# Performance work log

Hardware: AMD Instinct MI355X
Metric: run time of the kernel (lower is better)

Reference implementation:

```python
import jax, jax.numpy as jnp
import numpy as np

N_AGENTS = 32
BROADCAST = 1
HIDDEN = 64
R, T = 16, 512
D_IN = (N_AGENTS - 1) * (3 + BROADCAST)  # 124
D_OUT = 2 + BROADCAST  # 3


def setup_inputs() -> dict:
    key = jax.random.key(0)
    ks = jax.random.split(key, 8)
    runs = jax.random.normal(ks[0], (R, T, N_AGENTS, N_AGENTS - 1, 3), jnp.float32)
    # init_comm(): uniform(1, 2) of shape (broadcast, N) per run
    comm_init = jax.random.uniform(ks[1], (R, BROADCAST, N_AGENTS), jnp.float32, 1.0, 2.0)
    scale = 0.05  # keep tanh out of saturation
    w1 = jax.random.normal(ks[2], (HIDDEN, D_IN), jnp.float32) * scale
    b1 = jax.random.normal(ks[3], (HIDDEN,), jnp.float32) * scale
    w2 = jax.random.normal(ks[4], (HIDDEN, HIDDEN), jnp.float32) * scale
    b2 = jax.random.normal(ks[5], (HIDDEN,), jnp.float32) * scale
    w3 = jax.random.normal(ks[6], (D_OUT, HIDDEN), jnp.float32) * scale
    b3 = jax.random.normal(ks[7], (D_OUT,), jnp.float32) * scale
    return {"runs": runs, "comm_init": comm_init, "w1": w1, "b1": b1,
            "w2": w2, "b2": b2, "w3": w3, "b3": b3}


def reference(runs, comm_init, w1, b1, w2, b2, w3, b3):
    # runs: [R, T, N, N-1, 3]; comm_init: [R, broadcast, N]
    Rr, Tt, Nn = runs.shape[0], runs.shape[1], runs.shape[2]
    # skip_diag_strided: row i = all agent indices except i, in order
    n_closest = jnp.asarray(
        np.array([[j for j in range(Nn) if j != i] for i in range(Nn)]), jnp.int32)
    agent_ids = jnp.arange(Nn, dtype=jnp.int32)

    def snet(x):  # eval mode: dropout disabled
        h = jnp.tanh(x @ w1.T + b1)
        h = jnp.tanh(h @ w2.T + b2)
        return h @ w3.T + b3  # [2 + broadcast]

    def agent_step(comm, inp):
        xs_i, idx_i, i = inp  # xs_i: [N-1, 3], idx_i: [N-1]
        rel = comm[:, idx_i]  # [broadcast, N-1] gather of neighbor comm
        x = jnp.concatenate([xs_i.reshape(-1), rel.reshape(-1)])  # [D_IN]
        out = snet(x)
        # comm update is detached in torch (output[2:].detach().numpy())
        comm = comm.at[:, i].set(jax.lax.stop_gradient(out[2:]))
        return comm, out[:2]

    def t_step(comm, xs_t):  # sequential scatter-update across agents
        comm, ctrl = jax.lax.scan(agent_step, comm, (xs_t, n_closest, agent_ids))
        return comm, ctrl  # ctrl: [N, 2]

    def run_fn(run, c0):
        _, controls = jax.lax.scan(t_step, c0, run)  # [T, N, 2]
        return controls

    return jax.vmap(run_fn)(runs, comm_init)  # [R, T, N, 2]
```

## Files before the change

kernel.cpp:

```cpp
#include <hip/hip_runtime.h>


#define R_RUNS 16
#define T_STEPS 512
#define NA 32
#define HID 64
#define XS 93
#define DIN 124
#define STEPS_PER_RUN (T_STEPS * NA)
#define RTI_TOT (R_RUNS * STEPS_PER_RUN)

#define PRE1_OFF 65536
#define WS_NEEDED ((size_t)PRE1_OFF + (size_t)RTI_TOT * HID * 4 + 4096)

typedef _Float16 half2_t __attribute__((ext_vector_type(2)));
typedef unsigned int uint2v __attribute__((ext_vector_type(2)));

#if defined(__has_builtin)
#if __has_builtin(__builtin_amdgcn_permlane16_swap) && __has_builtin(__builtin_amdgcn_permlane32_swap)
#define HAVE_PLSWAP 1
#endif
#endif
#ifndef HAVE_PLSWAP
#define HAVE_PLSWAP 0
#endif

#if defined(__has_builtin)
#if __has_builtin(__builtin_amdgcn_exp2f)
#define EXPFN(x) __builtin_amdgcn_exp2f(x)
#define SC 2.8853900817779268f
#define HAVE_EXP2 1
#endif
#endif
#ifndef HAVE_EXP2
#define EXPFN(x) __expf(x)
#define SC 2.0f
#define HAVE_EXP2 0
#endif

__device__ __forceinline__ float fast_tanh(float x) {
  float e = __expf(2.f * x);
  return fmaf(-2.f, __builtin_amdgcn_rcpf(e + 1.f), 1.f);
}

__device__ __forceinline__ float dot2h(half2_t a, half2_t b, float c) {
#if __has_builtin(__builtin_amdgcn_fdot2)
  return __builtin_amdgcn_fdot2(a, b, c, false);
#else
  return fmaf((float)a.x, (float)b.x, fmaf((float)a.y, (float)b.y, c));
#endif
}

__device__ __forceinline__ half2_t bch(unsigned u) {
  return __builtin_bit_cast(half2_t, u);
}

#define DPP_ADD(x, ctrl, rmask) \
  (x) += __int_as_float(__builtin_amdgcn_update_dpp(0, __float_as_int(x), (ctrl), (rmask), 0xf, true))

__device__ __forceinline__ float wave64_sum_bcast(float x) {
  DPP_ADD(x, 0x111, 0xf);
  DPP_ADD(x, 0x112, 0xf);
  DPP_ADD(x, 0x114, 0xf);
  DPP_ADD(x, 0x118, 0xf);
  DPP_ADD(x, 0x142, 0xa);
  DPP_ADD(x, 0x143, 0xc);
  return __int_as_float(__builtin_amdgcn_readlane(__float_as_int(x), 63));
}

__device__ __forceinline__ float wave64_sum_all(float x) {
  DPP_ADD(x, 0xB1, 0xf);
  DPP_ADD(x, 0x4E, 0xf);
  DPP_ADD(x, 0x141, 0xf);
  DPP_ADD(x, 0x140, 0xf);
#if HAVE_PLSWAP
  uint2v p = __builtin_amdgcn_permlane16_swap(__float_as_uint(x), __float_as_uint(x), false, false);
  x = __uint_as_float(p[0]) + __uint_as_float(p[1]);
  p = __builtin_amdgcn_permlane32_swap(__float_as_uint(x), __float_as_uint(x), false, false);
  x = __uint_as_float(p[0]) + __uint_as_float(p[1]);
  return x;
#else
  DPP_ADD(x, 0x142, 0xa);
  DPP_ADD(x, 0x143, 0xc);
  return __int_as_float(__builtin_amdgcn_readlane(__float_as_int(x), 63));
#endif
}

__global__ void transpose_w1(const float* __restrict__ w1, float* __restrict__ w1T) {
  int idx = blockIdx.x * blockDim.x + threadIdx.x;
  if (idx < XS * HID) {
    int k = idx / HID, h = idx % HID;
    w1T[idx] = w1[h * DIN + k];
  }
}

__global__ __launch_bounds__(256) void pre1_kernel(
    const float* __restrict__ runs, const float* __restrict__ w1T,
    const float* __restrict__ b1, float* __restrict__ pre1) {
  const int wid = (blockIdx.x * 256 + threadIdx.x) >> 6;
  const int lane = threadIdx.x & 63;
  const float* xs = runs + (size_t)wid * XS;
  float a0 = b1[lane], a1 = 0.f, a2 = 0.f;
#pragma unroll 4
  for (int k = 0; k < 31; ++k) {
    a0 = fmaf(xs[3 * k],     w1T[(3 * k) * HID + lane],     a0);
    a1 = fmaf(xs[3 * k + 1], w1T[(3 * k + 1) * HID + lane], a1);
    a2 = fmaf(xs[3 * k + 2], w1T[(3 * k + 2) * HID + lane], a2);
  }
  pre1[(size_t)wid * HID + lane] = SC * ((a0 + a1) + a2);
}

__global__ __launch_bounds__(256) void out_kernel(
    const float* __restrict__ h2, const float* __restrict__ w3,
    const float* __restrict__ b3, float* __restrict__ out) {
  const int rti = blockIdx.x * 256 + threadIdx.x;
  const float4* hv4 = (const float4*)(h2 + (size_t)rti * HID);
  const float4* w0v = (const float4*)w3;
  const float4* w1v = (const float4*)(w3 + HID);
  float p00 = 0.f, p01 = 0.f, p02 = 0.f, p03 = 0.f;
  float p10 = 0.f, p11 = 0.f, p12 = 0.f, p13 = 0.f;
#pragma unroll
  for (int k = 0; k < 16; ++k) {
    float4 hv = hv4[k];
    float4 w0 = w0v[k];
    float4 w1r = w1v[k];
    p00 = fmaf(w0.x, hv.x, p00);  p01 = fmaf(w0.y, hv.y, p01);
    p02 = fmaf(w0.z, hv.z, p02);  p03 = fmaf(w0.w, hv.w, p03);
    p10 = fmaf(w1r.x, hv.x, p10); p11 = fmaf(w1r.y, hv.y, p11);
    p12 = fmaf(w1r.z, hv.z, p12); p13 = fmaf(w1r.w, hv.w, p13);
  }
  float o0 = ((p00 + p01) + (p02 + p03)) + b3[0];
  float o1 = ((p10 + p11) + (p12 + p13)) + b3[1];
  *(float2*)(out + (size_t)rti * 2) = make_float2(o0, o1);
}

__global__ __launch_bounds__(64, 1) void seq_kernel(
    const float* __restrict__ w1, const float* __restrict__ w2,
    const float* __restrict__ b2, const float* __restrict__ w3,
    const float* __restrict__ b3, const float* __restrict__ comm_init,
    float* pre1h2) {
  const int h = threadIdx.x;
  const int r = blockIdx.x;
  const int hb = h * 33;

  __shared__ float Asl[HID * 33];
  __shared__ float Bsl[HID * 33];
  __shared__ __align__(16) float commL[NA];
  __shared__ __align__(16) _Float16 h1s16[HID];
  __shared__ __align__(16) float pbuf[2][2048 + 64];

  for (int j = 0; j < 31; ++j) Asl[hb + j] = SC * w1[h * DIN + 93 + j];
  Asl[hb + 31] = 0.f;
  Asl[hb + 32] = 0.f;
  Bsl[hb] = 0.f;
  for (int j = 1; j < 32; ++j) Bsl[hb + j] = SC * w1[h * DIN + 92 + j];
  Bsl[hb + 32] = 0.f;

  const float4* w2v = (const float4*)(w2 + h * HID);
  const float4 r0 = w2v[0],  r1 = w2v[1],  r2 = w2v[2],  r3 = w2v[3];
  const float4 r4 = w2v[4],  r5 = w2v[5],  r6 = w2v[6],  r7 = w2v[7];
  const float4 r8 = w2v[8],  r9 = w2v[9],  r10 = w2v[10], r11 = w2v[11];
  const float4 r12 = w2v[12], r13 = w2v[13], r14 = w2v[14], r15 = w2v[15];
#define PK2S(n, f4) \
  const half2_t n##a = {(_Float16)(SC * (f4).x), (_Float16)(SC * (f4).y)}; \
  const half2_t n##b = {(_Float16)(SC * (f4).z), (_Float16)(SC * (f4).w)}
  PK2S(q0, r0);  PK2S(q1, r1);  PK2S(q2, r2);  PK2S(q3, r3);
  PK2S(q4, r4);  PK2S(q5, r5);  PK2S(q6, r6);  PK2S(q7, r7);
  PK2S(q8, r8);  PK2S(q9, r9);  PK2S(q10, r10); PK2S(q11, r11);
  PK2S(q12, r12); PK2S(q13, r13); PK2S(q14, r14); PK2S(q15, r15);
#undef PK2S

  const float b2s = SC * b2[h];
  const float w32h = w3[2 * HID + h];
  const float w32n2 = -2.f * w32h;
  const float b32 = b3[2];

  float commR = (h < NA) ? comm_init[r * NA + h] : 0.f;
  if (h < NA) commL[h] = commR;

  float* prow = pre1h2 + (size_t)r * STEPS_PER_RUN * HID;

  {
    const float4* s0 = (const float4*)prow;
    const float4* s1 = (const float4*)(prow + 2048);
    float4* d0 = (float4*)&pbuf[0][0];
    float4* d1 = (float4*)&pbuf[1][0];
#pragma unroll
    for (int j = 0; j < 8; ++j) d0[j * 64 + h] = s0[j * 64 + h];
#pragma unroll
    for (int j = 0; j < 8; ++j) d1[j * 64 + h] = s1[j * 64 + h];
  }

  for (int t = 0; t < T_STEPS; ++t) {
    float* pb = pbuf[t & 1];
    int tk = (t + 2 <= T_STEPS - 1) ? t + 2 : T_STEPS - 1;
    const float4* gsrc = (const float4*)(prow + (size_t)tk * 2048);
    float4 g0 = gsrc[0 * 64 + h], g1 = gsrc[1 * 64 + h];
    float4 g2 = gsrc[2 * 64 + h], g3 = gsrc[3 * 64 + h];
    float4 g4 = gsrc[4 * 64 + h], g5 = gsrc[5 * 64 + h];
    float4 g6 = gsrc[6 * 64 + h], g7 = gsrc[7 * 64 + h];

    const float4* cv4 = (const float4*)commL;
    float f0 = 0.f, f1 = 0.f, f2 = 0.f, f3 = 0.f;
#pragma unroll
    for (int q = 0; q < 8; ++q) {
      float4 c = cv4[q];
      f0 = fmaf(Bsl[hb + 4 * q + 0], c.x, f0);
      f1 = fmaf(Bsl[hb + 4 * q + 1], c.y, f1);
      f2 = fmaf(Bsl[hb + 4 * q + 2], c.z, f2);
      f3 = fmaf(Bsl[hb + 4 * q + 3], c.w, f3);
    }
    const float FB2 = (f0 + f1) + (f2 + f3);
    const float c0s = commR;
    float Q2 = 0.f, S2 = 0.f;
    float A2_c = Asl[hb];
    float E = pb[h] + FB2;
    float* h2t = prow + (size_t)t * 2048;

#pragma unroll 4
    for (int i = 0; i < NA; ++i) {
      float pf2_n = pb[(i + 1) * 64 + h];
      float A2_n = Asl[hb + i + 1];
      float B2_n = Bsl[hb + i + 1];
      float old_n = __int_as_float(__builtin_amdgcn_readlane(__float_as_int(c0s), i + 1));
      float e1 = EXPFN(E);
      float r1v = __builtin_amdgcn_rcpf(e1 + 1.f);
      float h1 = fmaf(-2.f, r1v, 1.f);
      h1s16[h] = (_Float16)h1;
      float S2n = fmaf(B2_n, old_n, S2);
      float Qb2 = fmaf(A2_c, b32, Q2);
      float H = pf2_n + (FB2 - S2n) + Qb2;
      const uint4* hv = (const uint4*)h1s16;
      uint4 X0 = hv[0], X1 = hv[1], X2 = hv[2], X3 = hv[3];
      uint4 X4 = hv[4], X5 = hv[5], X6 = hv[6], X7 = hv[7];
      float a0 = b2s, a1 = 0.f, a2 = 0.f, a3 = 0.f;
#define DOTB(Xq, qe, qo) \
      a0 = dot2h(qe##a, bch(Xq.x), a0); a1 = dot2h(qe##b, bch(Xq.y), a1); \
      a2 = dot2h(qo##a, bch(Xq.z), a2); a3 = dot2h(qo##b, bch(Xq.w), a3)
      DOTB(X0, q0, q1);   DOTB(X1, q2, q3);
      DOTB(X2, q4, q5);   DOTB(X3, q6, q7);
      DOTB(X4, q8, q9);   DOTB(X5, q10, q11);
      DOTB(X6, q12, q13); DOTB(X7, q14, q15);
#undef DOTB
      float y2 = (a0 + a1) + (a2 + a3);
      float e2 = EXPFN(y2);
      float r2v = __builtin_amdgcn_rcpf(e2 + 1.f);
      float xr = fmaf(w32n2, r2v, w32h);
      float csum = wave64_sum_all(xr);
      float h2v = fmaf(-2.f, r2v, 1.f);
      h2t[i * 64 + h] = h2v;
      float c_new = csum + b32;
      commR = (h == i) ? c_new : commR;
      E = fmaf(A2_c, csum, H);
      Q2 = fmaf(A2_c, csum, Qb2);
      S2 = S2n; A2_c = A2_n;
    }
    if (h < NA) commL[h] = commR;
    float4* pd = (float4*)pb;
    pd[0 * 64 + h] = g0; pd[1 * 64 + h] = g1;
    pd[2 * 64 + h] = g2; pd[3 * 64 + h] = g3;
    pd[4 * 64 + h] = g4; pd[5 * 64 + h] = g5;
    pd[6 * 64 + h] = g6; pd[7 * 64 + h] = g7;
  }
}

__global__ __launch_bounds__(64, 1) void seq_fused(
    const float* __restrict__ runs, const float* __restrict__ comm_init,
    const float* __restrict__ w1, const float* __restrict__ b1,
    const float* __restrict__ w2, const float* __restrict__ b2,
    const float* __restrict__ w3, const float* __restrict__ b3,
    float* __restrict__ out) {
  const int r = blockIdx.x;
  const int h = threadIdx.x;
  const int hb = h * 33;

  __shared__ float Asl[HID * 33];
  __shared__ float Bsl[HID * 33];
  __shared__ float commL[NA];
  __shared__ __align__(16) float h1s[HID];
  __shared__ float w1xs[XS * HID];
  __shared__ __align__(16) float xsl[96];

  for (int j = 0; j < 31; ++j) Asl[hb + j] = w1[h * DIN + 93 + j];
  Asl[hb + 31] = 0.f;
  Bsl[hb] = 0.f;
  for (int j = 1; j < 32; ++j) Bsl[hb + j] = w1[h * DIN + 92 + j];
  for (int k = 0; k < XS; ++k) w1xs[k * HID + h] = w1[h * DIN + k];

  float w2r[HID];
#pragma unroll
  for (int k = 0; k < HID; ++k) w2r[k] = w2[h * HID + k];
  const float b1h = b1[h];
  const float b2h = b2[h];
  const float w30h = w3[h], w31h = w3[HID + h], w32h = w3[2 * HID + h];
  const float b30 = b3[0], b31 = b3[1], b32 = b3[2];
  if (h < NA) commL[h] = comm_init[r * NA + h];

  const float* xbase = runs + (size_t)r * STEPS_PER_RUN * XS;
  float xa = xbase[h];
  float xb = (h < XS - 64) ? xbase[64 + h] : 0.f;
  float* outp = out + (size_t)r * STEPS_PER_RUN * 2;
  __syncthreads();

  int s = 0;
  for (int t = 0; t < T_STEPS; ++t) {
    float FB = 0.f;
#pragma unroll
    for (int j = 0; j < NA; ++j) FB = fmaf(Bsl[hb + j], commL[j], FB);
    float Q = 0.f, S = 0.f;
    for (int i = 0; i < NA; ++i, ++s) {
      int sn = s + 1; if (sn > STEPS_PER_RUN - 1) sn = STEPS_PER_RUN - 1;
      const float* xn = xbase + (size_t)sn * XS;
      xsl[h] = xa;
      if (h < XS - 64) xsl[64 + h] = xb;
      __syncthreads();
      float xa_n = xn[h];
      float xb_n = (h < XS - 64) ? xn[64 + h] : 0.f;
      float a0 = b1h, a1 = 0.f, a2 = 0.f;
#pragma unroll 4
      for (int k = 0; k < 31; ++k) {
        a0 = fmaf(xsl[3 * k],     w1xs[(3 * k) * HID + h],     a0);
        a1 = fmaf(xsl[3 * k + 1], w1xs[(3 * k + 1) * HID + h], a1);
        a2 = fmaf(xsl[3 * k + 2], w1xs[(3 * k + 2) * HID + h], a2);
      }
      float old_i = commL[i];
      S = fmaf(Bsl[hb + i], old_i, S);
      float h1 = fast_tanh(((a0 + a1) + a2) + FB + Q - S);
      h1s[h] = h1;
      __syncthreads();
      float c0 = b2h, c1 = 0.f, c2 = 0.f, c3 = 0.f;
      const float4* hv4 = (const float4*)h1s;
#pragma unroll
      for (int k4 = 0; k4 < 16; ++k4) {
        float4 hv = hv4[k4];
        c0 = fmaf(w2r[4 * k4 + 0], hv.x, c0);
        c1 = fmaf(w2r[4 * k4 + 1], hv.y, c1);
        c2 = fmaf(w2r[4 * k4 + 2], hv.z, c2);
        c3 = fmaf(w2r[4 * k4 + 3], hv.w, c3);
      }
      float h2 = fast_tanh((c0 + c1) + (c2 + c3));
      float o0 = wave64_sum_bcast(w30h * h2) + b30;
      float o1 = wave64_sum_bcast(w31h * h2) + b31;
      float c_new = wave64_sum_bcast(w32h * h2) + b32;
      if (h == 0) *(float2*)(outp + (size_t)s * 2) = make_float2(o0, o1);
      Q = fmaf(Asl[hb + i], c_new, Q);
      if (h == i) commL[h] = c_new;
      __syncthreads();
      xa = xa_n; xb = xb_n;
    }
  }
}

extern "C" void kernel_launch(void* const* d_in, const int* in_sizes, int n_in,
                              void* d_out, int out_size, void* d_ws, size_t ws_size,
                              hipStream_t stream) {
  const float* runs = (const float*)d_in[0];
  const float* comm_init = (const float*)d_in[1];
  const float* w1 = (const float*)d_in[2];
  const float* b1 = (const float*)d_in[3];
  const float* w2 = (const float*)d_in[4];
  const float* b2 = (const float*)d_in[5];
  const float* w3 = (const float*)d_in[6];
  const float* b3 = (const float*)d_in[7];
  float* out = (float*)d_out;

  if (ws_size >= WS_NEEDED) {
    float* w1T = (float*)d_ws;
    float* pre1 = (float*)((char*)d_ws + PRE1_OFF);
    hipLaunchKernelGGL(transpose_w1, dim3((XS * HID + 255) / 256), dim3(256), 0, stream,
                       w1, w1T);
    hipLaunchKernelGGL(pre1_kernel, dim3(RTI_TOT / 4), dim3(256), 0, stream,
                       runs, w1T, b1, pre1);
    hipLaunchKernelGGL(seq_kernel, dim3(R_RUNS), dim3(64), 0, stream,
                       w1, w2, b2, w3, b3, comm_init, pre1);
    hipLaunchKernelGGL(out_kernel, dim3(RTI_TOT / 256), dim3(256), 0, stream,
                       pre1, w3, b3, out);
  } else {
    hipLaunchKernelGGL(seq_fused, dim3(R_RUNS), dim3(64), 0, stream,
                       runs, comm_init, w1, b1, w2, b2, w3, b3, out);
  }
}
```

Measured before the change: 4.348 ms.

## Split layer-2 matvec across wave halves with permlane swap; batch pre1 rows

In the sequential kernel, each lane now computes partial dot products over only 32 of the 64 hidden inputs for two output rows: its own and its partner lane's (h^32). The halves are then combined with a permlane32 swap. This halves the per-step LDS reads of h1, the main cost on the serial critical path, in exchange for one cross-lane swap. Separately, the pre1 kernel keeps a float4-packed transposed w1 in registers and processes four rows per wave, which raises register use.

```diff
diff --git a/kernel.cpp b/kernel.cpp
--- a/kernel.cpp
+++ b/kernel.cpp
@@ -86,28 +86,41 @@
 #endif
 }
 
-__global__ void transpose_w1(const float* __restrict__ w1, float* __restrict__ w1T) {
+__global__ void transpose_w1(const float* __restrict__ w1, float* __restrict__ w1T4) {
   int idx = blockIdx.x * blockDim.x + threadIdx.x;
-  if (idx < XS * HID) {
-    int k = idx / HID, h = idx % HID;
-    w1T[idx] = w1[h * DIN + k];
-  }
-}
-
+  if (idx < 24 * HID * 4) {
+    int c = idx & 3, h = (idx >> 2) & 63, kk = idx >> 8;
+    int k = 4 * kk + c;
+    w1T4[idx] = (k < XS) ? w1[h * DIN + k] : 0.f;
+  }
+}
+
+#define PRE1_BATCH 4
 __global__ __launch_bounds__(256) void pre1_kernel(
-    const float* __restrict__ runs, const float* __restrict__ w1T,
+    const float* __restrict__ runs, const float* __restrict__ w1T4,
     const float* __restrict__ b1, float* __restrict__ pre1) {
   const int wid = (blockIdx.x * 256 + threadIdx.x) >> 6;
   const int lane = threadIdx.x & 63;
-  const float* xs = runs + (size_t)wid * XS;
-  float a0 = b1[lane], a1 = 0.f, a2 = 0.f;
-#pragma unroll 4
-  for (int k = 0; k < 31; ++k) {
-    a0 = fmaf(xs[3 * k],     w1T[(3 * k) * HID + lane],     a0);
-    a1 = fmaf(xs[3 * k + 1], w1T[(3 * k + 1) * HID + lane], a1);
-    a2 = fmaf(xs[3 * k + 2], w1T[(3 * k + 2) * HID + lane], a2);
-  }
-  pre1[(size_t)wid * HID + lane] = SC * ((a0 + a1) + a2);
+  const int rti0 = wid * PRE1_BATCH;
+  const float4* wv = (const float4*)w1T4;
+  float4 w[24];
+#pragma unroll
+  for (int kk = 0; kk < 24; ++kk) w[kk] = wv[kk * 64 + lane];
+  const float b1s = b1[lane];
+#pragma unroll
+  for (int u = 0; u < PRE1_BATCH; ++u) {
+    const float* xs = runs + (size_t)(rti0 + u) * XS;
+    float a0 = b1s, a1 = 0.f, a2 = 0.f, a3 = 0.f;
+#pragma unroll
+    for (int kk = 0; kk < 23; ++kk) {
+      a0 = fmaf(xs[4 * kk + 0], w[kk].x, a0);
+      a1 = fmaf(xs[4 * kk + 1], w[kk].y, a1);
+      a2 = fmaf(xs[4 * kk + 2], w[kk].z, a2);
+      a3 = fmaf(xs[4 * kk + 3], w[kk].w, a3);
+    }
+    a0 = fmaf(xs[92], w[23].x, a0);
+    pre1[(size_t)(rti0 + u) * HID + lane] = SC * ((a0 + a1) + (a2 + a3));
+  }
 }
 
 __global__ __launch_bounds__(256) void out_kernel(
@@ -156,6 +169,23 @@
   for (int j = 1; j < 32; ++j) Bsl[hb + j] = SC * w1[h * DIN + 92 + j];
   Bsl[hb + 32] = 0.f;
 
+#if HAVE_PLSWAP
+  const int hi = h >> 5;
+  const float4* wA = (const float4*)(w2 + h * HID + hi * 32);
+  const float4* wB = (const float4*)(w2 + (h ^ 32) * HID + hi * 32);
+  const float4 A0 = wA[0], A1 = wA[1], A2v = wA[2], A3 = wA[3];
+  const float4 A4 = wA[4], A5 = wA[5], A6 = wA[6], A7 = wA[7];
+  const float4 B0 = wB[0], B1 = wB[1], B2v = wB[2], B3 = wB[3];
+  const float4 B4 = wB[4], B5 = wB[5], B6 = wB[6], B7 = wB[7];
+#define PK2S(n, f4) \
+  const half2_t n##a = {(_Float16)(SC * (f4).x), (_Float16)(SC * (f4).y)}; \
+  const half2_t n##b = {(_Float16)(SC * (f4).z), (_Float16)(SC * (f4).w)}
+  PK2S(pa0, A0); PK2S(pa1, A1); PK2S(pa2, A2v); PK2S(pa3, A3);
+  PK2S(pa4, A4); PK2S(pa5, A5); PK2S(pa6, A6);  PK2S(pa7, A7);
+  PK2S(pb0, B0); PK2S(pb1, B1); PK2S(pb2, B2v); PK2S(pb3, B3);
+  PK2S(pb4, B4); PK2S(pb5, B5); PK2S(pb6, B6);  PK2S(pb7, B7);
+#undef PK2S
+#else
   const float4* w2v = (const float4*)(w2 + h * HID);
   const float4 r0 = w2v[0],  r1 = w2v[1],  r2 = w2v[2],  r3 = w2v[3];
   const float4 r4 = w2v[4],  r5 = w2v[5],  r6 = w2v[6],  r7 = w2v[7];
@@ -169,6 +199,7 @@
   PK2S(q8, r8);  PK2S(q9, r9);  PK2S(q10, r10); PK2S(q11, r11);
   PK2S(q12, r12); PK2S(q13, r13); PK2S(q14, r14); PK2S(q15, r15);
 #undef PK2S
+#endif
 
   const float b2s = SC * b2[h];
   const float w32h = w3[2 * HID + h];
@@ -230,6 +261,26 @@
       float S2n = fmaf(B2_n, old_n, S2);
       float Qb2 = fmaf(A2_c, b32, Q2);
       float H = pf2_n + (FB2 - S2n) + Qb2;
+      float y2;
+#if HAVE_PLSWAP
+      const uint4* hv = (const uint4*)h1s16;
+      uint4 X0 = hv[hi * 4 + 0], X1 = hv[hi * 4 + 1];
+      uint4 X2 = hv[hi * 4 + 2], X3 = hv[hi * 4 + 3];
+      float a0 = b2s, a1 = 0.f, a2 = 0.f, a3 = 0.f;
+#define DOTP(Xq, e, o) \
+      a0 = dot2h(pa##e##a, bch(Xq.x), a0); a2 = dot2h(pb##e##a, bch(Xq.x), a2); \
+      a1 = dot2h(pa##e##b, bch(Xq.y), a1); a3 = dot2h(pb##e##b, bch(Xq.y), a3); \
+      a0 = dot2h(pa##o##a, bch(Xq.z), a0); a2 = dot2h(pb##o##a, bch(Xq.z), a2); \
+      a1 = dot2h(pa##o##b, bch(Xq.w), a1); a3 = dot2h(pb##o##b, bch(Xq.w), a3)
+      DOTP(X0, 0, 1); DOTP(X1, 2, 3); DOTP(X2, 4, 5); DOTP(X3, 6, 7);
+#undef DOTP
+      float pA = a0 + a1;
+      float pBo = a2 + a3;
+      uint2v sw = __builtin_amdgcn_permlane32_swap(
+          __float_as_uint(pBo), __float_as_uint(pBo), false, false);
+      float pB = hi ? __uint_as_float(sw[0]) : __uint_as_float(sw[1]);
+      y2 = pA + pB;
+#else
       const uint4* hv = (const uint4*)h1s16;
       uint4 X0 = hv[0], X1 = hv[1], X2 = hv[2], X3 = hv[3];
       uint4 X4 = hv[4], X5 = hv[5], X6 = hv[6], X7 = hv[7];
@@ -242,7 +293,8 @@
       DOTB(X4, q8, q9);   DOTB(X5, q10, q11);
       DOTB(X6, q12, q13); DOTB(X7, q14, q15);
 #undef DOTB
-      float y2 = (a0 + a1) + (a2 + a3);
+      y2 = (a0 + a1) + (a2 + a3);
+#endif
       float e2 = EXPFN(y2);
       float r2v = __builtin_amdgcn_rcpf(e2 + 1.f);
       float xr = fmaf(w32n2, r2v, w32h);
@@ -365,12 +417,12 @@
   float* out = (float*)d_out;
 
   if (ws_size >= WS_NEEDED) {
-    float* w1T = (float*)d_ws;
+    float* w1T4 = (float*)d_ws;
     float* pre1 = (float*)((char*)d_ws + PRE1_OFF);
-    hipLaunchKernelGGL(transpose_w1, dim3((XS * HID + 255) / 256), dim3(256), 0, stream,
-                       w1, w1T);
-    hipLaunchKernelGGL(pre1_kernel, dim3(RTI_TOT / 4), dim3(256), 0, stream,
-                       runs, w1T, b1, pre1);
+    hipLaunchKernelGGL(transpose_w1, dim3((24 * HID * 4 + 255) / 256), dim3(256), 0, stream,
+                       w1, w1T4);
+    hipLaunchKernelGGL(pre1_kernel, dim3(RTI_TOT / (PRE1_BATCH * 4)), dim3(256), 0, stream,
+                       runs, w1T4, b1, pre1);
     hipLaunchKernelGGL(seq_kernel, dim3(R_RUNS), dim3(64), 0, stream,
                        w1, w2, b2, w3, b3, comm_init, pre1);
     hipLaunchKernelGGL(out_kernel, dim3(RTI_TOT / 256), dim3(256), 0, stream,
```

New measurement: 4.321 ms. About the same (-0.6%).
